# Kernel optimization log

Measured on AMD Instinct MI355X. Metric: run time of the kernel, lower is better.

The kernel has to match this reference:

```python
import jax, jax.numpy as jnp
import numpy as np

N_NODES = 100000


def gcn_conv(x, W, b, src, dst, num_nodes):
    # PyG GCNConv: h = x @ W; out_i = sum_j norm_ij * h_j + b
    # with self-loops already appended to (src, dst) and
    # norm_ij = deg^{-1/2}[src] * deg^{-1/2}[dst].
    h = x @ W  # [N, out]
    deg = jax.ops.segment_sum(jnp.ones_like(src, dtype=h.dtype), dst, num_segments=num_nodes)
    dinv = jnp.where(deg > 0, jax.lax.rsqrt(deg), 0.0)
    norm = dinv[src] * dinv[dst]  # [E]
    msg = h[src] * norm[:, None]  # [E, out]  (gather + scale)
    out = jax.ops.segment_sum(msg, dst, num_segments=num_nodes)  # scatter-add
    return out + b


def setup_inputs() -> dict:
    key = jax.random.key(0)
    ks = jax.random.split(key, 8)
    x = jax.random.normal(ks[0], (N_NODES, 3), dtype=jnp.float32)
    edge_index = jax.random.randint(ks[1], (2, 3200000), 0, N_NODES, dtype=jnp.int64)

    def glorot(k, fan_in, fan_out):
        s = jnp.sqrt(6.0 / (fan_in + fan_out))
        return jax.random.uniform(k, (fan_in, fan_out), jnp.float32, -s, s)

    W1 = glorot(ks[2], 3, 16)
    b1 = jnp.zeros((16,), jnp.float32)
    W2 = glorot(ks[3], 16, 32)
    b2 = jnp.zeros((32,), jnp.float32)
    W3 = glorot(ks[4], 32, 2)
    b3 = jnp.zeros((2,), jnp.float32)
    return {"x": x, "edge_index": edge_index, "W1": W1, "b1": b1,
            "W2": W2, "b2": b2, "W3": W3, "b3": b3}


def reference(x, edge_index, W1, b1, W2, b2, W3, b3):
    num_nodes = x.shape[0]
    # add self-loops once (GCNConv default add_self_loops=True)
    loops = jnp.arange(num_nodes, dtype=edge_index.dtype)
    src = jnp.concatenate([edge_index[0], loops])
    dst = jnp.concatenate([edge_index[1], loops])

    h = jax.nn.relu(gcn_conv(x, W1, b1, src, dst, num_nodes))
    h = jax.nn.relu(gcn_conv(h, W2, b2, src, dst, num_nodes))
    return gcn_conv(h, W3, b3, src, dst, num_nodes)
```

## Files before the change

### kernel.cpp

```cpp
#include <hip/hip_runtime.h>

static constexpr int NND = 100000;
static constexpr int NED = 3200000;
static constexpr int NB  = (NND + 255) / 256;
static constexpr int NCHUNK = 256;
static constexpr int EPC = NED / NCHUNK;
static constexpr int SCAN_N = NB * NCHUNK;


__global__ void k_hist(const int* __restrict__ dst, int* __restrict__ counts) {
    __shared__ int h[NB];
    for (int i = threadIdx.x; i < NB; i += 256) h[i] = 0;
    __syncthreads();
    int c = blockIdx.x;
    int base = c * EPC;
    for (int i = threadIdx.x; i < EPC; i += 256)
        atomicAdd(&h[dst[base + i] >> 8], 1);
    __syncthreads();
    for (int b = threadIdx.x; b < NB; b += 256)
        counts[b * NCHUNK + c] = h[b];
}


__global__ void k_scan1(const int* __restrict__ in, int* __restrict__ excl,
                        int* __restrict__ blockSums, int n) {
    __shared__ int lds[256];
    int tid = threadIdx.x;
    int base = blockIdx.x * 1024 + tid * 4;
    int v[4]; int sum = 0;
#pragma unroll
    for (int k = 0; k < 4; ++k) { int idx = base + k; v[k] = (idx < n) ? in[idx] : 0; sum += v[k]; }
    lds[tid] = sum; __syncthreads();
    for (int off = 1; off < 256; off <<= 1) {
        int x = lds[tid];
        int y = (tid >= off) ? lds[tid - off] : 0;
        __syncthreads();
        lds[tid] = x + y;
        __syncthreads();
    }
    int run = lds[tid] - sum;
#pragma unroll
    for (int k = 0; k < 4; ++k) { int idx = base + k; if (idx < n) excl[idx] = run; run += v[k]; }
    if (tid == 0) blockSums[blockIdx.x] = lds[255];
}

__global__ void k_scan2(int* __restrict__ blockSums, int nb) {
    __shared__ int lds[128];
    int tid = threadIdx.x;
    int v = (tid < nb) ? blockSums[tid] : 0;
    lds[tid] = v; __syncthreads();
    for (int off = 1; off < 128; off <<= 1) {
        int x = lds[tid];
        int y = (tid >= off) ? lds[tid - off] : 0;
        __syncthreads();
        lds[tid] = x + y;
        __syncthreads();
    }
    if (tid < nb) blockSums[tid] = lds[tid] - v;
}

__global__ void k_scan3(int* __restrict__ excl, const int* __restrict__ blockSums,
                        int n, int e) {
    int i = blockIdx.x * blockDim.x + threadIdx.x;
    if (i < n) excl[i] += blockSums[i >> 10];
    if (i == n) excl[n] = e;
}


__global__ void k_part(const int* __restrict__ src, const int* __restrict__ dst,
                       const int* __restrict__ excl, int* __restrict__ tmp) {
    __shared__ int cur[NB];
    int c = blockIdx.x;
    for (int b = threadIdx.x; b < NB; b += 256) cur[b] = excl[b * NCHUNK + c];
    __syncthreads();
    int base = c * EPC;
    for (int i = threadIdx.x; i < EPC; i += 256) {
        int d = dst[base + i];
        int s = src[base + i];
        int b = d >> 8;
        int pos = atomicAdd(&cur[b], 1);
        tmp[pos] = s | ((d & 255) << 20);
    }
}


__global__ void k_bucket(const int* __restrict__ excl, const int* __restrict__ tmp,
                         int* __restrict__ ssrc, int* __restrict__ rowptr,
                         float* __restrict__ dinv) {
    __shared__ int cnt[256];
    __shared__ int lds[256];
    int b = blockIdx.x, t = threadIdx.x;
    int start = excl[b * NCHUNK];
    int end   = excl[(b + 1) * NCHUNK];
    cnt[t] = 0;
    __syncthreads();
    for (int i = start + t; i < end; i += 256)
        atomicAdd(&cnt[tmp[i] >> 20], 1);
    __syncthreads();
    int v = cnt[t];
    lds[t] = v; __syncthreads();
    for (int off = 1; off < 256; off <<= 1) {
        int x = lds[t];
        int y = (t >= off) ? lds[t - off] : 0;
        __syncthreads();
        lds[t] = x + y;
        __syncthreads();
    }
    int node = b * 256 + t;
    int rp = start + lds[t] - v;
    if (node < NND) {
        rowptr[node] = rp;
        dinv[node] = rsqrtf((float)(v + 1));
    }
    if (b == 0 && t == 0) rowptr[NND] = NED;
    cnt[t] = rp;
    __syncthreads();
    for (int i = start + t; i < end; i += 256) {
        int p = tmp[i];
        int pos = atomicAdd(&cnt[p >> 20], 1);
        ssrc[pos] = p & 0xFFFFF;
    }
}


__global__ void k_prep1(const float* __restrict__ x, const float* __restrict__ dinv,
                        float4* __restrict__ t4, int n) {
    int i = blockIdx.x * blockDim.x + threadIdx.x;
    if (i >= n) return;
    float d = dinv[i];
    const float* xr = x + (size_t)i * 3;
    t4[i] = make_float4(xr[0] * d, xr[1] * d, xr[2] * d, 0.f);
}


__global__ void k_g4mm1(const int* __restrict__ rowptr, const int* __restrict__ ssrc,
                        const float4* __restrict__ t4, const float* __restrict__ dinv,
                        const float* __restrict__ W1, const float* __restrict__ b1,
                        float* __restrict__ t16, int n) {
    __shared__ float sW[48];
    __shared__ float sb[16];
    if (threadIdx.x < 48) sW[threadIdx.x] = W1[threadIdx.x];
    if (threadIdx.x < 16) sb[threadIdx.x] = b1[threadIdx.x];
    __syncthreads();
    int node = blockIdx.x * blockDim.x + threadIdx.x;
    if (node >= n) return;

    float4 a = t4[node];
    float a0 = a.x, a1 = a.y, a2 = a.z;
    int beg = rowptr[node], end = rowptr[node + 1];
    constexpr int U = 8;
    int j = beg;
    for (; j + U <= end; j += U) {
        int s[U];
#pragma unroll
        for (int k = 0; k < U; ++k) s[k] = ssrc[j + k];
        float4 v[U];
#pragma unroll
        for (int k = 0; k < U; ++k) v[k] = t4[s[k]];
#pragma unroll
        for (int k = 0; k < U; ++k) { a0 += v[k].x; a1 += v[k].y; a2 += v[k].z; }
    }
    for (; j < end; ++j) {
        float4 v = t4[ssrc[j]];
        a0 += v.x; a1 += v.y; a2 += v.z;
    }
    float d = dinv[node];
    float p0 = a0 * d, p1 = a1 * d, p2 = a2 * d;
    float* orow = t16 + (size_t)node * 16;
#pragma unroll
    for (int q = 0; q < 4; ++q) {
        float4 o;
        float* op = reinterpret_cast<float*>(&o);
#pragma unroll
        for (int r = 0; r < 4; ++r) {
            int jj = q * 4 + r;
            float h = fmaf(p0, sW[jj], fmaf(p1, sW[16 + jj], fmaf(p2, sW[32 + jj], sb[jj])));
            op[r] = fmaxf(h, 0.f) * d;
        }
        *reinterpret_cast<float4*>(orow + q * 4) = o;
    }
}


__global__ void k_g16u(const int* __restrict__ rowptr, const int* __restrict__ ssrc,
                       const float* __restrict__ t16, const float* __restrict__ dinv,
                       float* __restrict__ u16, int n) {
    constexpr int TPN = 4, U = 8;
    int i = blockIdx.x * blockDim.x + threadIdx.x;
    int node = i / TPN;
    int fv = i % TPN;
    if (node >= n) return;
    int f0 = fv * 4;

    float4 acc = *reinterpret_cast<const float4*>(t16 + (size_t)node * 16 + f0);
    int beg = rowptr[node], end = rowptr[node + 1];
    int j = beg;
    for (; j + U <= end; j += U) {
        int s[U];
#pragma unroll
        for (int k = 0; k < U; ++k) s[k] = ssrc[j + k];
        float4 v[U];
#pragma unroll
        for (int k = 0; k < U; ++k)
            v[k] = *reinterpret_cast<const float4*>(t16 + (size_t)s[k] * 16 + f0);
#pragma unroll
        for (int k = 0; k < U; ++k) {
            acc.x += v[k].x; acc.y += v[k].y; acc.z += v[k].z; acc.w += v[k].w;
        }
    }
    for (; j < end; ++j) {
        float4 v = *reinterpret_cast<const float4*>(t16 + (size_t)ssrc[j] * 16 + f0);
        acc.x += v.x; acc.y += v.y; acc.z += v.z; acc.w += v.w;
    }
    float d = dinv[node];
    acc.x *= d; acc.y *= d; acc.z *= d; acc.w *= d;
    *reinterpret_cast<float4*>(u16 + (size_t)node * 16 + f0) = acc;
}


__global__ void k_mm23(const float* __restrict__ u16, const float* __restrict__ W2,
                       const float* __restrict__ b2, const float* __restrict__ W3,
                       const float* __restrict__ dinv, float2* __restrict__ t3, int n) {
    __shared__ float sW2[512];
    __shared__ float sb2[32];
    __shared__ float sW3[64];
    for (int i = threadIdx.x; i < 512; i += 256) sW2[i] = W2[i];
    if (threadIdx.x < 32) sb2[threadIdx.x] = b2[threadIdx.x];
    if (threadIdx.x < 64) sW3[threadIdx.x] = W3[threadIdx.x];
    __syncthreads();
    int node = blockIdx.x * blockDim.x + threadIdx.x;
    if (node >= n) return;
    float u[16];
#pragma unroll
    for (int q = 0; q < 4; ++q) {
        float4 v = *reinterpret_cast<const float4*>(u16 + (size_t)node * 16 + q * 4);
        u[q * 4 + 0] = v.x; u[q * 4 + 1] = v.y; u[q * 4 + 2] = v.z; u[q * 4 + 3] = v.w;
    }
    float t30 = 0.f, t31 = 0.f;
#pragma unroll
    for (int jj = 0; jj < 32; ++jj) {
        float h = sb2[jj];
#pragma unroll
        for (int k = 0; k < 16; ++k) h = fmaf(u[k], sW2[k * 32 + jj], h);
        h = fmaxf(h, 0.f);
        t30 = fmaf(h, sW3[jj * 2 + 0], t30);
        t31 = fmaf(h, sW3[jj * 2 + 1], t31);
    }
    float d = dinv[node];
    t3[node] = make_float2(t30 * d, t31 * d);
}


__global__ void k_g2(const int* __restrict__ rowptr, const int* __restrict__ ssrc,
                     const float2* __restrict__ t3, const float* __restrict__ dinv,
                     const float* __restrict__ b3, float2* __restrict__ out, int n) {
    constexpr int U = 8;
    int node = blockIdx.x * blockDim.x + threadIdx.x;
    if (node >= n) return;
    float2 t = t3[node];
    float a0 = t.x, a1 = t.y;
    int beg = rowptr[node], end = rowptr[node + 1];
    int j = beg;
    for (; j + U <= end; j += U) {
        int s[U];
#pragma unroll
        for (int k = 0; k < U; ++k) s[k] = ssrc[j + k];
        float2 v[U];
#pragma unroll
        for (int k = 0; k < U; ++k) v[k] = t3[s[k]];
#pragma unroll
        for (int k = 0; k < U; ++k) { a0 += v[k].x; a1 += v[k].y; }
    }
    for (; j < end; ++j) {
        float2 v = t3[ssrc[j]];
        a0 += v.x; a1 += v.y;
    }
    float d = dinv[node];
    out[node] = make_float2(fmaf(d, a0, b3[0]), fmaf(d, a1, b3[1]));
}


static inline size_t align256(size_t x) { return (x + 255) & ~(size_t)255; }

extern "C" void kernel_launch(void* const* d_in, const int* in_sizes, int n_in,
                              void* d_out, int out_size, void* d_ws, size_t ws_size,
                              hipStream_t stream) {
    const float* x  = (const float*)d_in[0];
    const int*   ei = (const int*)d_in[1];
    const float* W1 = (const float*)d_in[2];
    const float* b1 = (const float*)d_in[3];
    const float* W2 = (const float*)d_in[4];
    const float* b2 = (const float*)d_in[5];
    const float* W3 = (const float*)d_in[6];
    const float* b3 = (const float*)d_in[7];
    float2* out = (float2*)d_out;

    const int* src = ei;
    const int* dst = ei + NED;

    char* p = (char*)d_ws;
    float* dinv   = (float*)p; p += align256(sizeof(float) * (size_t)NND);
    int*   rowptr = (int*)p;   p += align256(sizeof(int) * (size_t)(NND + 1));
    int*   excl   = (int*)p;   p += align256(sizeof(int) * (size_t)(SCAN_N + 1));
    int*   bsums  = (int*)p;   p += align256(sizeof(int) * 128);
    int*   ssrc   = (int*)p;   p += align256(sizeof(int) * (size_t)NED);
    float4* t4    = (float4*)p; p += align256(sizeof(float4) * (size_t)NND);
    float2* t3    = (float2*)p; p += align256(sizeof(float2) * (size_t)NND);
    float* regA   = (float*)p; p += align256(sizeof(float) * (size_t)NND * 32);
    int*   tmp    = (int*)regA;
    float* t16    = regA;
    float* u16    = regA + (size_t)NND * 16;

    const int B = 256;
    const int gridN = (NND + B - 1) / B;
    const int nScanBlocks = (SCAN_N + 1023) / 1024;

    k_hist<<<NCHUNK, B, 0, stream>>>(dst, excl);
    k_scan1<<<nScanBlocks, 256, 0, stream>>>(excl, excl, bsums, SCAN_N);
    k_scan2<<<1, 128, 0, stream>>>(bsums, nScanBlocks);
    k_scan3<<<(SCAN_N + 1 + B - 1) / B, B, 0, stream>>>(excl, bsums, SCAN_N, NED);
    k_part<<<NCHUNK, B, 0, stream>>>(src, dst, excl, tmp);
    k_bucket<<<NB, B, 0, stream>>>(excl, tmp, ssrc, rowptr, dinv);

    k_prep1<<<gridN, B, 0, stream>>>(x, dinv, t4, NND);
    k_g4mm1<<<gridN, B, 0, stream>>>(rowptr, ssrc, t4, dinv, W1, b1, t16, NND);

    k_g16u<<<(NND * 4 + B - 1) / B, B, 0, stream>>>(rowptr, ssrc, t16, dinv, u16, NND);
    k_mm23<<<gridN, B, 0, stream>>>(u16, W2, b2, W3, dinv, t3, NND);

    k_g2<<<gridN, B, 0, stream>>>(rowptr, ssrc, t3, dinv, b3, out, NND);
}
```

Before: 168.2 us.

## Split 16-wide gather into two 8-wide passes and fuse prep and mm23

Folds the x*dinv prep into the bucket kernel and drops the separate prep launch. The 16-feature layer-2 aggregation is split into two 8-feature tables, each gathered in its own pass. The second pass is fused with the W2/W3 matmul, with the two lanes of a node exchanging halves through shuffles. Each gather pass touches a smaller table, which should improve cache hit rates on the random gathers, but the edge index list is now read twice and the workspace is packed into the tmp region.

```diff
diff --git a/kernel.cpp b/kernel.cpp
--- a/kernel.cpp
+++ b/kernel.cpp
@@ -86,7 +86,8 @@
 
 __global__ void k_bucket(const int* __restrict__ excl, const int* __restrict__ tmp,
                          int* __restrict__ ssrc, int* __restrict__ rowptr,
-                         float* __restrict__ dinv) {
+                         float* __restrict__ dinv, const float* __restrict__ x,
+                         float4* __restrict__ t4) {
     __shared__ int cnt[256];
     __shared__ int lds[256];
     int b = blockIdx.x, t = threadIdx.x;
@@ -100,17 +101,20 @@
     int v = cnt[t];
     lds[t] = v; __syncthreads();
     for (int off = 1; off < 256; off <<= 1) {
-        int x = lds[t];
+        int xv = lds[t];
         int y = (t >= off) ? lds[t - off] : 0;
         __syncthreads();
-        lds[t] = x + y;
+        lds[t] = xv + y;
         __syncthreads();
     }
     int node = b * 256 + t;
     int rp = start + lds[t] - v;
     if (node < NND) {
         rowptr[node] = rp;
-        dinv[node] = rsqrtf((float)(v + 1));
+        float d = rsqrtf((float)(v + 1));
+        dinv[node] = d;
+        const float* xr = x + (size_t)node * 3;
+        t4[node] = make_float4(xr[0] * d, xr[1] * d, xr[2] * d, 0.f);
     }
     if (b == 0 && t == 0) rowptr[NND] = NED;
     cnt[t] = rp;
@@ -123,20 +127,10 @@
 }
 
 
-__global__ void k_prep1(const float* __restrict__ x, const float* __restrict__ dinv,
-                        float4* __restrict__ t4, int n) {
-    int i = blockIdx.x * blockDim.x + threadIdx.x;
-    if (i >= n) return;
-    float d = dinv[i];
-    const float* xr = x + (size_t)i * 3;
-    t4[i] = make_float4(xr[0] * d, xr[1] * d, xr[2] * d, 0.f);
-}
-
-
 __global__ void k_g4mm1(const int* __restrict__ rowptr, const int* __restrict__ ssrc,
                         const float4* __restrict__ t4, const float* __restrict__ dinv,
                         const float* __restrict__ W1, const float* __restrict__ b1,
-                        float* __restrict__ t16, int n) {
+                        float* __restrict__ t16a, float* __restrict__ t16b, int n) {
     __shared__ float sW[48];
     __shared__ float sb[16];
     if (threadIdx.x < 48) sW[threadIdx.x] = W1[threadIdx.x];
@@ -166,33 +160,30 @@
     }
     float d = dinv[node];
     float p0 = a0 * d, p1 = a1 * d, p2 = a2 * d;
-    float* orow = t16 + (size_t)node * 16;
-#pragma unroll
-    for (int q = 0; q < 4; ++q) {
-        float4 o;
-        float* op = reinterpret_cast<float*>(&o);
-#pragma unroll
-        for (int r = 0; r < 4; ++r) {
-            int jj = q * 4 + r;
-            float h = fmaf(p0, sW[jj], fmaf(p1, sW[16 + jj], fmaf(p2, sW[32 + jj], sb[jj])));
-            op[r] = fmaxf(h, 0.f) * d;
-        }
-        *reinterpret_cast<float4*>(orow + q * 4) = o;
-    }
-}
-
-
-__global__ void k_g16u(const int* __restrict__ rowptr, const int* __restrict__ ssrc,
-                       const float* __restrict__ t16, const float* __restrict__ dinv,
-                       float* __restrict__ u16, int n) {
-    constexpr int TPN = 4, U = 8;
+    float h[16];
+#pragma unroll
+    for (int jj = 0; jj < 16; ++jj) {
+        float hv = fmaf(p0, sW[jj], fmaf(p1, sW[16 + jj], fmaf(p2, sW[32 + jj], sb[jj])));
+        h[jj] = fmaxf(hv, 0.f) * d;
+    }
+    float* ra = t16a + (size_t)node * 8;
+    float* rb = t16b + (size_t)node * 8;
+    *reinterpret_cast<float4*>(ra)     = make_float4(h[0], h[1], h[2], h[3]);
+    *reinterpret_cast<float4*>(ra + 4) = make_float4(h[4], h[5], h[6], h[7]);
+    *reinterpret_cast<float4*>(rb)     = make_float4(h[8], h[9], h[10], h[11]);
+    *reinterpret_cast<float4*>(rb + 4) = make_float4(h[12], h[13], h[14], h[15]);
+}
+
+
+__global__ void k_g8(const int* __restrict__ rowptr, const int* __restrict__ ssrc,
+                     const float* __restrict__ tab, const float* __restrict__ dinv,
+                     float* __restrict__ u, int n) {
+    constexpr int U = 8;
     int i = blockIdx.x * blockDim.x + threadIdx.x;
-    int node = i / TPN;
-    int fv = i % TPN;
+    int node = i >> 1;
+    int f0 = (i & 1) * 4;
     if (node >= n) return;
-    int f0 = fv * 4;
-
-    float4 acc = *reinterpret_cast<const float4*>(t16 + (size_t)node * 16 + f0);
+    float4 acc = *reinterpret_cast<const float4*>(tab + (size_t)node * 8 + f0);
     int beg = rowptr[node], end = rowptr[node + 1];
     int j = beg;
     for (; j + U <= end; j += U) {
@@ -202,25 +193,27 @@
         float4 v[U];
 #pragma unroll
         for (int k = 0; k < U; ++k)
-            v[k] = *reinterpret_cast<const float4*>(t16 + (size_t)s[k] * 16 + f0);
+            v[k] = *reinterpret_cast<const float4*>(tab + (size_t)s[k] * 8 + f0);
 #pragma unroll
         for (int k = 0; k < U; ++k) {
             acc.x += v[k].x; acc.y += v[k].y; acc.z += v[k].z; acc.w += v[k].w;
         }
     }
     for (; j < end; ++j) {
-        float4 v = *reinterpret_cast<const float4*>(t16 + (size_t)ssrc[j] * 16 + f0);
+        float4 v = *reinterpret_cast<const float4*>(tab + (size_t)ssrc[j] * 8 + f0);
         acc.x += v.x; acc.y += v.y; acc.z += v.z; acc.w += v.w;
     }
     float d = dinv[node];
     acc.x *= d; acc.y *= d; acc.z *= d; acc.w *= d;
-    *reinterpret_cast<float4*>(u16 + (size_t)node * 16 + f0) = acc;
-}
-
-
-__global__ void k_mm23(const float* __restrict__ u16, const float* __restrict__ W2,
-                       const float* __restrict__ b2, const float* __restrict__ W3,
-                       const float* __restrict__ dinv, float2* __restrict__ t3, int n) {
+    *reinterpret_cast<float4*>(u + (size_t)node * 8 + f0) = acc;
+}
+
+
+__global__ void k_g8mm(const int* __restrict__ rowptr, const int* __restrict__ ssrc,
+                       const float* __restrict__ tabB, const float* __restrict__ u8a,
+                       const float* __restrict__ dinv,
+                       const float* __restrict__ W2, const float* __restrict__ b2,
+                       const float* __restrict__ W3, float2* __restrict__ t3, int n) {
     __shared__ float sW2[512];
     __shared__ float sb2[32];
     __shared__ float sW3[64];
@@ -228,26 +221,67 @@
     if (threadIdx.x < 32) sb2[threadIdx.x] = b2[threadIdx.x];
     if (threadIdx.x < 64) sW3[threadIdx.x] = W3[threadIdx.x];
     __syncthreads();
-    int node = blockIdx.x * blockDim.x + threadIdx.x;
+
+    constexpr int U = 8;
+    int i = blockIdx.x * blockDim.x + threadIdx.x;
+    int node = i >> 1;
+    int half = i & 1;
+    int f0 = half * 4;
     if (node >= n) return;
-    float u[16];
-#pragma unroll
-    for (int q = 0; q < 4; ++q) {
-        float4 v = *reinterpret_cast<const float4*>(u16 + (size_t)node * 16 + q * 4);
-        u[q * 4 + 0] = v.x; u[q * 4 + 1] = v.y; u[q * 4 + 2] = v.z; u[q * 4 + 3] = v.w;
+
+    float4 acc = *reinterpret_cast<const float4*>(tabB + (size_t)node * 8 + f0);
+    int beg = rowptr[node], end = rowptr[node + 1];
+    int j = beg;
+    for (; j + U <= end; j += U) {
+        int s[U];
+#pragma unroll
+        for (int k = 0; k < U; ++k) s[k] = ssrc[j + k];
+        float4 v[U];
+#pragma unroll
+        for (int k = 0; k < U; ++k)
+            v[k] = *reinterpret_cast<const float4*>(tabB + (size_t)s[k] * 8 + f0);
+#pragma unroll
+        for (int k = 0; k < U; ++k) {
+            acc.x += v[k].x; acc.y += v[k].y; acc.z += v[k].z; acc.w += v[k].w;
+        }
+    }
+    for (; j < end; ++j) {
+        float4 v = *reinterpret_cast<const float4*>(tabB + (size_t)ssrc[j] * 8 + f0);
+        acc.x += v.x; acc.y += v.y; acc.z += v.z; acc.w += v.w;
+    }
+    float d = dinv[node];
+    float up[4] = {acc.x * d, acc.y * d, acc.z * d, acc.w * d};
+    float4 lo4 = *reinterpret_cast<const float4*>(u8a + (size_t)node * 8 + f0);
+    float lo[4] = {lo4.x, lo4.y, lo4.z, lo4.w};
+    float plo[4], pup[4];
+#pragma unroll
+    for (int c = 0; c < 4; ++c) {
+        plo[c] = __shfl_xor(lo[c], 1);
+        pup[c] = __shfl_xor(up[c], 1);
+    }
+    float uu[16];
+#pragma unroll
+    for (int c = 0; c < 4; ++c) {
+        uu[c]      = half ? plo[c] : lo[c];
+        uu[4 + c]  = half ? lo[c]  : plo[c];
+        uu[8 + c]  = half ? pup[c] : up[c];
+        uu[12 + c] = half ? up[c]  : pup[c];
     }
     float t30 = 0.f, t31 = 0.f;
-#pragma unroll
-    for (int jj = 0; jj < 32; ++jj) {
+    int jbase = half * 16;
+#pragma unroll
+    for (int r = 0; r < 16; ++r) {
+        int jj = jbase + r;
         float h = sb2[jj];
 #pragma unroll
-        for (int k = 0; k < 16; ++k) h = fmaf(u[k], sW2[k * 32 + jj], h);
+        for (int k = 0; k < 16; ++k) h = fmaf(uu[k], sW2[k * 32 + jj], h);
         h = fmaxf(h, 0.f);
         t30 = fmaf(h, sW3[jj * 2 + 0], t30);
         t31 = fmaf(h, sW3[jj * 2 + 1], t31);
     }
-    float d = dinv[node];
-    t3[node] = make_float2(t30 * d, t31 * d);
+    t30 += __shfl_xor(t30, 1);
+    t31 += __shfl_xor(t31, 1);
+    if (half == 0) t3[node] = make_float2(t30 * d, t31 * d);
 }
 
 
@@ -306,13 +340,15 @@
     int*   ssrc   = (int*)p;   p += align256(sizeof(int) * (size_t)NED);
     float4* t4    = (float4*)p; p += align256(sizeof(float4) * (size_t)NND);
     float2* t3    = (float2*)p; p += align256(sizeof(float2) * (size_t)NND);
-    float* regA   = (float*)p; p += align256(sizeof(float) * (size_t)NND * 32);
-    int*   tmp    = (int*)regA;
-    float* t16    = regA;
-    float* u16    = regA + (size_t)NND * 16;
+    char*  q      = p;         p += align256(sizeof(int) * (size_t)NED);
+    int*   tmp    = (int*)q;
+    float* t16a   = (float*)q;
+    float* t16b   = t16a + (size_t)NND * 8;
+    float* u8a    = t16b + (size_t)NND * 8;
 
     const int B = 256;
     const int gridN = (NND + B - 1) / B;
+    const int grid2N = (NND * 2 + B - 1) / B;
     const int nScanBlocks = (SCAN_N + 1023) / 1024;
 
     k_hist<<<NCHUNK, B, 0, stream>>>(dst, excl);
@@ -320,13 +356,12 @@
     k_scan2<<<1, 128, 0, stream>>>(bsums, nScanBlocks);
     k_scan3<<<(SCAN_N + 1 + B - 1) / B, B, 0, stream>>>(excl, bsums, SCAN_N, NED);
     k_part<<<NCHUNK, B, 0, stream>>>(src, dst, excl, tmp);
-    k_bucket<<<NB, B, 0, stream>>>(excl, tmp, ssrc, rowptr, dinv);
-
-    k_prep1<<<gridN, B, 0, stream>>>(x, dinv, t4, NND);
-    k_g4mm1<<<gridN, B, 0, stream>>>(rowptr, ssrc, t4, dinv, W1, b1, t16, NND);
-
-    k_g16u<<<(NND * 4 + B - 1) / B, B, 0, stream>>>(rowptr, ssrc, t16, dinv, u16, NND);
-    k_mm23<<<gridN, B, 0, stream>>>(u16, W2, b2, W3, dinv, t3, NND);
+    k_bucket<<<NB, B, 0, stream>>>(excl, tmp, ssrc, rowptr, dinv, x, t4);
+
+    k_g4mm1<<<gridN, B, 0, stream>>>(rowptr, ssrc, t4, dinv, W1, b1, t16a, t16b, NND);
+
+    k_g8<<<grid2N, B, 0, stream>>>(rowptr, ssrc, t16a, dinv, u8a, NND);
+    k_g8mm<<<grid2N, B, 0, stream>>>(rowptr, ssrc, t16b, u8a, dinv, W2, b2, W3, t3, NND);
 
     k_g2<<<gridN, B, 0, stream>>>(rowptr, ssrc, t3, dinv, b3, out, NND);
 }
```

New measurement: 181.9 us. 1.08x slower.

## Fuse layer-2 gather with dense MLP, fold prep into bucket, vectorize edge loads

Applied to the files above, without the earlier changes.

Merges the 16-wide gather and the layer-2/3 dense transform into one kernel. Four threads per node exchange their partial feature vectors with shuffles, each computes 8 of the 32 hidden units, and a shuffle reduction combines the results. This removes the u16 intermediate round trip and one launch. The x*dinv prep step is folded into the bucket kernel, which removes another launch. Edge histogram and partition now use int4 vector loads plus nontemporal loads and stores. The workspace shrinks because u16 is gone.

```diff
diff --git a/kernel.cpp b/kernel.cpp
--- a/kernel.cpp
+++ b/kernel.cpp
@@ -7,15 +7,22 @@
 static constexpr int EPC = NED / NCHUNK;
 static constexpr int SCAN_N = NB * NCHUNK;
 
+typedef int int4n __attribute__((ext_vector_type(4)));
+
 
 __global__ void k_hist(const int* __restrict__ dst, int* __restrict__ counts) {
     __shared__ int h[NB];
     for (int i = threadIdx.x; i < NB; i += 256) h[i] = 0;
     __syncthreads();
     int c = blockIdx.x;
-    int base = c * EPC;
-    for (int i = threadIdx.x; i < EPC; i += 256)
-        atomicAdd(&h[dst[base + i] >> 8], 1);
+    const int4n* d4 = reinterpret_cast<const int4n*>(dst + c * EPC);
+    for (int i = threadIdx.x; i < EPC / 4; i += 256) {
+        int4n v = d4[i];
+        atomicAdd(&h[v.x >> 8], 1);
+        atomicAdd(&h[v.y >> 8], 1);
+        atomicAdd(&h[v.z >> 8], 1);
+        atomicAdd(&h[v.w >> 8], 1);
+    }
     __syncthreads();
     for (int b = threadIdx.x; b < NB; b += 256)
         counts[b * NCHUNK + c] = h[b];
@@ -73,20 +80,27 @@
     int c = blockIdx.x;
     for (int b = threadIdx.x; b < NB; b += 256) cur[b] = excl[b * NCHUNK + c];
     __syncthreads();
-    int base = c * EPC;
-    for (int i = threadIdx.x; i < EPC; i += 256) {
-        int d = dst[base + i];
-        int s = src[base + i];
-        int b = d >> 8;
-        int pos = atomicAdd(&cur[b], 1);
-        tmp[pos] = s | ((d & 255) << 20);
+    const int4n* s4 = reinterpret_cast<const int4n*>(src + c * EPC);
+    const int4n* d4 = reinterpret_cast<const int4n*>(dst + c * EPC);
+    for (int i = threadIdx.x; i < EPC / 4; i += 256) {
+        int4n sv = __builtin_nontemporal_load(&s4[i]);
+        int4n dv = __builtin_nontemporal_load(&d4[i]);
+        int ss[4] = {sv.x, sv.y, sv.z, sv.w};
+        int dd[4] = {dv.x, dv.y, dv.z, dv.w};
+#pragma unroll
+        for (int k = 0; k < 4; ++k) {
+            int b = dd[k] >> 8;
+            int pos = atomicAdd(&cur[b], 1);
+            __builtin_nontemporal_store(ss[k] | ((dd[k] & 255) << 20), &tmp[pos]);
+        }
     }
 }
 
 
 __global__ void k_bucket(const int* __restrict__ excl, const int* __restrict__ tmp,
                          int* __restrict__ ssrc, int* __restrict__ rowptr,
-                         float* __restrict__ dinv) {
+                         float* __restrict__ dinv, const float* __restrict__ x,
+                         float4* __restrict__ t4) {
     __shared__ int cnt[256];
     __shared__ int lds[256];
     int b = blockIdx.x, t = threadIdx.x;
@@ -95,41 +109,34 @@
     cnt[t] = 0;
     __syncthreads();
     for (int i = start + t; i < end; i += 256)
-        atomicAdd(&cnt[tmp[i] >> 20], 1);
+        atomicAdd(&cnt[__builtin_nontemporal_load(&tmp[i]) >> 20], 1);
     __syncthreads();
     int v = cnt[t];
     lds[t] = v; __syncthreads();
     for (int off = 1; off < 256; off <<= 1) {
-        int x = lds[t];
+        int xv = lds[t];
         int y = (t >= off) ? lds[t - off] : 0;
         __syncthreads();
-        lds[t] = x + y;
+        lds[t] = xv + y;
         __syncthreads();
     }
     int node = b * 256 + t;
     int rp = start + lds[t] - v;
     if (node < NND) {
         rowptr[node] = rp;
-        dinv[node] = rsqrtf((float)(v + 1));
+        float d = rsqrtf((float)(v + 1));
+        dinv[node] = d;
+        const float* xr = x + (size_t)node * 3;
+        t4[node] = make_float4(xr[0] * d, xr[1] * d, xr[2] * d, 0.f);
     }
     if (b == 0 && t == 0) rowptr[NND] = NED;
     cnt[t] = rp;
     __syncthreads();
     for (int i = start + t; i < end; i += 256) {
-        int p = tmp[i];
+        int p = __builtin_nontemporal_load(&tmp[i]);
         int pos = atomicAdd(&cnt[p >> 20], 1);
         ssrc[pos] = p & 0xFFFFF;
     }
-}
-
-
-__global__ void k_prep1(const float* __restrict__ x, const float* __restrict__ dinv,
-                        float4* __restrict__ t4, int n) {
-    int i = blockIdx.x * blockDim.x + threadIdx.x;
-    if (i >= n) return;
-    float d = dinv[i];
-    const float* xr = x + (size_t)i * 3;
-    t4[i] = make_float4(xr[0] * d, xr[1] * d, xr[2] * d, 0.f);
 }
 
 
@@ -182,45 +189,10 @@
 }
 
 
-__global__ void k_g16u(const int* __restrict__ rowptr, const int* __restrict__ ssrc,
-                       const float* __restrict__ t16, const float* __restrict__ dinv,
-                       float* __restrict__ u16, int n) {
-    constexpr int TPN = 4, U = 8;
-    int i = blockIdx.x * blockDim.x + threadIdx.x;
-    int node = i / TPN;
-    int fv = i % TPN;
-    if (node >= n) return;
-    int f0 = fv * 4;
-
-    float4 acc = *reinterpret_cast<const float4*>(t16 + (size_t)node * 16 + f0);
-    int beg = rowptr[node], end = rowptr[node + 1];
-    int j = beg;
-    for (; j + U <= end; j += U) {
-        int s[U];
-#pragma unroll
-        for (int k = 0; k < U; ++k) s[k] = ssrc[j + k];
-        float4 v[U];
-#pragma unroll
-        for (int k = 0; k < U; ++k)
-            v[k] = *reinterpret_cast<const float4*>(t16 + (size_t)s[k] * 16 + f0);
-#pragma unroll
-        for (int k = 0; k < U; ++k) {
-            acc.x += v[k].x; acc.y += v[k].y; acc.z += v[k].z; acc.w += v[k].w;
-        }
-    }
-    for (; j < end; ++j) {
-        float4 v = *reinterpret_cast<const float4*>(t16 + (size_t)ssrc[j] * 16 + f0);
-        acc.x += v.x; acc.y += v.y; acc.z += v.z; acc.w += v.w;
-    }
-    float d = dinv[node];
-    acc.x *= d; acc.y *= d; acc.z *= d; acc.w *= d;
-    *reinterpret_cast<float4*>(u16 + (size_t)node * 16 + f0) = acc;
-}
-
-
-__global__ void k_mm23(const float* __restrict__ u16, const float* __restrict__ W2,
-                       const float* __restrict__ b2, const float* __restrict__ W3,
-                       const float* __restrict__ dinv, float2* __restrict__ t3, int n) {
+__global__ void k_g16mm(const int* __restrict__ rowptr, const int* __restrict__ ssrc,
+                        const float* __restrict__ t16, const float* __restrict__ dinv,
+                        const float* __restrict__ W2, const float* __restrict__ b2,
+                        const float* __restrict__ W3, float2* __restrict__ t3, int n) {
     __shared__ float sW2[512];
     __shared__ float sb2[32];
     __shared__ float sW3[64];
@@ -228,26 +200,67 @@
     if (threadIdx.x < 32) sb2[threadIdx.x] = b2[threadIdx.x];
     if (threadIdx.x < 64) sW3[threadIdx.x] = W3[threadIdx.x];
     __syncthreads();
-    int node = blockIdx.x * blockDim.x + threadIdx.x;
+
+    constexpr int U = 8;
+    int i = blockIdx.x * blockDim.x + threadIdx.x;
+    int node = i >> 2;
+    int fv = i & 3;
     if (node >= n) return;
-    float u[16];
-#pragma unroll
-    for (int q = 0; q < 4; ++q) {
-        float4 v = *reinterpret_cast<const float4*>(u16 + (size_t)node * 16 + q * 4);
-        u[q * 4 + 0] = v.x; u[q * 4 + 1] = v.y; u[q * 4 + 2] = v.z; u[q * 4 + 3] = v.w;
-    }
+    int f0 = fv * 4;
+
+    float4 acc = *reinterpret_cast<const float4*>(t16 + (size_t)node * 16 + f0);
+    int beg = rowptr[node], end = rowptr[node + 1];
+    int j = beg;
+    for (; j + U <= end; j += U) {
+        int s[U];
+#pragma unroll
+        for (int k = 0; k < U; ++k) s[k] = ssrc[j + k];
+        float4 v[U];
+#pragma unroll
+        for (int k = 0; k < U; ++k)
+            v[k] = *reinterpret_cast<const float4*>(t16 + (size_t)s[k] * 16 + f0);
+#pragma unroll
+        for (int k = 0; k < U; ++k) {
+            acc.x += v[k].x; acc.y += v[k].y; acc.z += v[k].z; acc.w += v[k].w;
+        }
+    }
+    for (; j < end; ++j) {
+        float4 v = *reinterpret_cast<const float4*>(t16 + (size_t)ssrc[j] * 16 + f0);
+        acc.x += v.x; acc.y += v.y; acc.z += v.z; acc.w += v.w;
+    }
+    float d = dinv[node];
+    float q[4] = {acc.x * d, acc.y * d, acc.z * d, acc.w * d};
+
+    float p1[4], p2[4], p3[4];
+#pragma unroll
+    for (int c = 0; c < 4; ++c) p1[c] = __shfl_xor(q[c], 1);
+#pragma unroll
+    for (int c = 0; c < 4; ++c) { p2[c] = __shfl_xor(q[c], 2); p3[c] = __shfl_xor(p1[c], 2); }
+
+    float uu[16];
+#pragma unroll
+    for (int c = 0; c < 4; ++c) {
+        uu[0 + c]  = fv == 0 ? q[c] : fv == 1 ? p1[c] : fv == 2 ? p2[c] : p3[c];
+        uu[4 + c]  = fv == 1 ? q[c] : fv == 0 ? p1[c] : fv == 3 ? p2[c] : p3[c];
+        uu[8 + c]  = fv == 2 ? q[c] : fv == 3 ? p1[c] : fv == 0 ? p2[c] : p3[c];
+        uu[12 + c] = fv == 3 ? q[c] : fv == 2 ? p1[c] : fv == 1 ? p2[c] : p3[c];
+    }
+
     float t30 = 0.f, t31 = 0.f;
-#pragma unroll
-    for (int jj = 0; jj < 32; ++jj) {
+    int jbase = fv * 8;
+#pragma unroll
+    for (int r = 0; r < 8; ++r) {
+        int jj = jbase + r;
         float h = sb2[jj];
 #pragma unroll
-        for (int k = 0; k < 16; ++k) h = fmaf(u[k], sW2[k * 32 + jj], h);
+        for (int k = 0; k < 16; ++k) h = fmaf(uu[k], sW2[k * 32 + jj], h);
         h = fmaxf(h, 0.f);
         t30 = fmaf(h, sW3[jj * 2 + 0], t30);
         t31 = fmaf(h, sW3[jj * 2 + 1], t31);
     }
-    float d = dinv[node];
-    t3[node] = make_float2(t30 * d, t31 * d);
+    t30 += __shfl_xor(t30, 1); t30 += __shfl_xor(t30, 2);
+    t31 += __shfl_xor(t31, 1); t31 += __shfl_xor(t31, 2);
+    if (fv == 0) t3[node] = make_float2(t30 * d, t31 * d);
 }
 
 
@@ -306,13 +319,13 @@
     int*   ssrc   = (int*)p;   p += align256(sizeof(int) * (size_t)NED);
     float4* t4    = (float4*)p; p += align256(sizeof(float4) * (size_t)NND);
     float2* t3    = (float2*)p; p += align256(sizeof(float2) * (size_t)NND);
-    float* regA   = (float*)p; p += align256(sizeof(float) * (size_t)NND * 32);
-    int*   tmp    = (int*)regA;
-    float* t16    = regA;
-    float* u16    = regA + (size_t)NND * 16;
+    char*  q      = p;         p += align256(sizeof(int) * (size_t)NED);
+    int*   tmp    = (int*)q;
+    float* t16    = (float*)q;
 
     const int B = 256;
     const int gridN = (NND + B - 1) / B;
+    const int grid4N = (NND * 4 + B - 1) / B;
     const int nScanBlocks = (SCAN_N + 1023) / 1024;
 
     k_hist<<<NCHUNK, B, 0, stream>>>(dst, excl);
@@ -320,13 +333,11 @@
     k_scan2<<<1, 128, 0, stream>>>(bsums, nScanBlocks);
     k_scan3<<<(SCAN_N + 1 + B - 1) / B, B, 0, stream>>>(excl, bsums, SCAN_N, NED);
     k_part<<<NCHUNK, B, 0, stream>>>(src, dst, excl, tmp);
-    k_bucket<<<NB, B, 0, stream>>>(excl, tmp, ssrc, rowptr, dinv);
-
-    k_prep1<<<gridN, B, 0, stream>>>(x, dinv, t4, NND);
+    k_bucket<<<NB, B, 0, stream>>>(excl, tmp, ssrc, rowptr, dinv, x, t4);
+
     k_g4mm1<<<gridN, B, 0, stream>>>(rowptr, ssrc, t4, dinv, W1, b1, t16, NND);
 
-    k_g16u<<<(NND * 4 + B - 1) / B, B, 0, stream>>>(rowptr, ssrc, t16, dinv, u16, NND);
-    k_mm23<<<gridN, B, 0, stream>>>(u16, W2, b2, W3, dinv, t3, NND);
+    k_g16mm<<<grid4N, B, 0, stream>>>(rowptr, ssrc, t16, dinv, W2, b2, W3, t3, NND);
 
     k_g2<<<gridN, B, 0, stream>>>(rowptr, ssrc, t3, dinv, b3, out, NND);
 }
```

After: 232.7 us. 38.4% more time.
